# Kernel tuning notes

Measured on AMD Instinct MI355X. Metric: run time of the kernel, lower is better.

## Reference

```python
import jax, jax.numpy as jnp
import numpy as np
from jax import lax

B, IMG, P, C_IN, E, H, NAX = 128, 224, 16, 1, 96, 4, 14
N = NAX * NAX  # 196 patches


def _ln(x, g, b, axes=(-1,)):
    mu = jnp.mean(x, axes, keepdims=True)
    v = jnp.var(x, axes, keepdims=True)
    return (x - mu) * lax.rsqrt(v + 1e-5) * g + b


def _embed3d(p):
    # p: [B, N, E]. Torch code rotates pair (2i,2i+1) by theta_i*col (row loop)
    # then theta_i*row (col loop) in-place => total angle theta_i*(row+col).
    bsz = p.shape[0]
    f = p.transpose(0, 2, 1).reshape(bsz, E, NAX, NAX)
    i = jnp.arange(E // 2, dtype=jnp.float32)
    theta = 10000.0 ** (-2.0 * i / E)  # [48]
    pos = jnp.arange(NAX, dtype=jnp.float32)
    ang = theta[:, None, None] * (pos[None, :, None] + pos[None, None, :])  # [48,14,14]
    cos, sin = jnp.cos(ang), jnp.sin(ang)
    xe, ye = f[:, 0::2], f[:, 1::2]  # [B,48,14,14] each
    rx = xe * cos - ye * sin
    ry = xe * sin + ye * cos
    f = jnp.stack([rx, ry], axis=2).reshape(bsz, E, NAX, NAX)  # re-interleave pairs
    return f.reshape(bsz, E, N).transpose(0, 2, 1)


def _mhsa(x, g, bt, Wqkv, bqkv, Wo, bo):
    # standard pre-norm residual MHSA block (MHSelfAttentionBlock assumed)
    h = _ln(x, g, bt)
    qkv = h @ Wqkv + bqkv  # [B,N,3E]
    q, k, v = jnp.split(qkv, 3, axis=-1)
    d = E // H
    def heads(t):
        return t.reshape(t.shape[0], N, H, d).transpose(0, 2, 1, 3)  # [B,H,N,d]
    q, k, v = heads(q), heads(k), heads(v)
    s = jnp.einsum('bhqd,bhkd->bhqk', q, k) / jnp.sqrt(jnp.float32(d))
    a = jax.nn.softmax(s, axis=-1)
    o = jnp.einsum('bhqk,bhkd->bhqd', a, v).transpose(0, 2, 1, 3).reshape(x.shape[0], N, E)
    return x + o @ Wo + bo


def _convT(x, w, b):
    # torch ConvTranspose2d(k=4, s=2, p=1); w: [C_in, C_out, 4, 4]
    wt = jnp.transpose(jnp.flip(w, (2, 3)), (1, 0, 2, 3))  # OIHW, flipped
    y = lax.conv_general_dilated(x, wt, (1, 1), ((2, 2), (2, 2)), lhs_dilation=(2, 2),
                                 dimension_numbers=('NCHW', 'OIHW', 'NCHW'))
    return y + b[None, :, None, None]


def _forward(x, timestep, Wp, bp, Wt1, bt1, Wt2, bt2,
             a0_g, a0_b, a0_Wqkv, a0_bqkv, a0_Wo, a0_bo,
             a1_g, a1_b, a1_Wqkv, a1_bqkv, a1_Wo, a1_bo,
             Wm0, bm0, Wm1, bm1, Wm2, bm2,
             Wd1, bd1, l1g, l1b, Wd2, bd2, l2g, l2b, Wd3, bd3, l3g, l3b, Wd4, bd4):
    # timestep embedding: emb = -log(0.5)*t -> [sin, cos] -> MLP
    e = 0.6931471805599453 * timestep[0]
    tv = jnp.stack([jnp.sin(e), jnp.cos(e)])  # [2]
    time = jax.nn.silu(tv @ Wt1 + bt1) @ Wt2 + bt2  # [E]
    # patch embed: conv stride 16
    p = lax.conv_general_dilated(x, Wp, (P, P), 'VALID',
                                 dimension_numbers=('NCHW', 'OIHW', 'NCHW'))
    p = (p + bp[None, :, None, None]).reshape(x.shape[0], E, N).transpose(0, 2, 1)  # [B,N,E]
    p = _embed3d(p)
    p = _mhsa(p, a0_g, a0_b, a0_Wqkv, a0_bqkv, a0_Wo, a0_bo)
    p = _mhsa(p, a1_g, a1_b, a1_Wqkv, a1_bqkv, a1_Wo, a1_bo)
    p = p + time
    p = jax.nn.silu(p @ Wm0 + bm0)
    p = jax.nn.silu(p @ Wm1 + bm1)
    p = jax.nn.silu(p @ Wm2 + bm2)
    # unpatchify decoder
    f = p.transpose(0, 2, 1).reshape(x.shape[0], E, NAX, NAX)
    f = jax.nn.silu(_ln(_convT(f, Wd1, bd1), l1g, l1b, (-2, -1)))  # [B,48,28,28]
    f = jax.nn.silu(_ln(_convT(f, Wd2, bd2), l2g, l2b, (-2, -1)))  # [B,24,56,56]
    f = jax.nn.silu(_ln(_convT(f, Wd3, bd3), l3g, l3b, (-2, -1)))  # [B,12,112,112]
    f = jax.nn.silu(_convT(f, Wd4, bd4))                            # [B,1,224,224]
    return jnp.clip(f, 0.0, 1.0)


def setup_inputs() -> dict:
    ks = jax.random.split(jax.random.key(0), 40)
    rn = lambda k, s: (jax.random.normal(k, s, jnp.float32) * 0.02)
    inp = {
        'x': jax.random.normal(ks[0], (B, C_IN, IMG, IMG), jnp.float32),
        'timestep': jax.random.uniform(ks[1], (1,), jnp.float32),
        'Wp': rn(ks[2], (E, C_IN, P, P)), 'bp': jnp.zeros((E,), jnp.float32),
        'Wt1': rn(ks[3], (2, 128)), 'bt1': jnp.zeros((128,), jnp.float32),
        'Wt2': rn(ks[4], (128, E)), 'bt2': jnp.zeros((E,), jnp.float32),
        'a0_g': jnp.ones((E,), jnp.float32), 'a0_b': jnp.zeros((E,), jnp.float32),
        'a0_Wqkv': rn(ks[5], (E, 3 * E)), 'a0_bqkv': jnp.zeros((3 * E,), jnp.float32),
        'a0_Wo': rn(ks[6], (E, E)), 'a0_bo': jnp.zeros((E,), jnp.float32),
        'a1_g': jnp.ones((E,), jnp.float32), 'a1_b': jnp.zeros((E,), jnp.float32),
        'a1_Wqkv': rn(ks[7], (E, 3 * E)), 'a1_bqkv': jnp.zeros((3 * E,), jnp.float32),
        'a1_Wo': rn(ks[8], (E, E)), 'a1_bo': jnp.zeros((E,), jnp.float32),
        'Wm0': rn(ks[9], (E, E)), 'bm0': jnp.zeros((E,), jnp.float32),
        'Wm1': rn(ks[10], (E, E)), 'bm1': jnp.zeros((E,), jnp.float32),
        'Wm2': rn(ks[11], (E, E)), 'bm2': jnp.zeros((E,), jnp.float32),
        'Wd1': rn(ks[12], (E, 48, 4, 4)), 'bd1': jnp.zeros((48,), jnp.float32),
        'l1g': jnp.ones((28, 28), jnp.float32), 'l1b': jnp.zeros((28, 28), jnp.float32),
        'Wd2': rn(ks[13], (48, 24, 4, 4)), 'bd2': jnp.zeros((24,), jnp.float32),
        'l2g': jnp.ones((56, 56), jnp.float32), 'l2b': jnp.zeros((56, 56), jnp.float32),
        'Wd3': rn(ks[14], (24, 12, 4, 4)), 'bd3': jnp.zeros((12,), jnp.float32),
        'l3g': jnp.ones((112, 112), jnp.float32), 'l3b': jnp.zeros((112, 112), jnp.float32),
        'Wd4': rn(ks[15], (12, 1, 4, 4)), 'bd4': jnp.zeros((1,), jnp.float32),
    }
    return inp


def reference(x, timestep, Wp, bp, Wt1, bt1, Wt2, bt2,
              a0_g, a0_b, a0_Wqkv, a0_bqkv, a0_Wo, a0_bo,
              a1_g, a1_b, a1_Wqkv, a1_bqkv, a1_Wo, a1_bo,
              Wm0, bm0, Wm1, bm1, Wm2, bm2,
              Wd1, bd1, l1g, l1b, Wd2, bd2, l2g, l2b, Wd3, bd3, l3g, l3b, Wd4, bd4):
    return _forward(x, timestep, Wp, bp, Wt1, bt1, Wt2, bt2,
                    a0_g, a0_b, a0_Wqkv, a0_bqkv, a0_Wo, a0_bo,
                    a1_g, a1_b, a1_Wqkv, a1_bqkv, a1_Wo, a1_bo,
                    Wm0, bm0, Wm1, bm1, Wm2, bm2,
                    Wd1, bd1, l1g, l1b, Wd2, bd2, l2g, l2b, Wd3, bd3, l3g, l3b, Wd4, bd4)
```

## Files before the change

kernel.cpp:

```cpp
#include <hip/hip_runtime.h>
#include <cmath>


#define B_   128
#define NPATCH 196
#define M_ROWS (B_*NPATCH)
#define E_   96

typedef _Float16 half8 __attribute__((ext_vector_type(8)));
typedef _Float16 half4v __attribute__((ext_vector_type(4)));
typedef _Float16 half2v __attribute__((ext_vector_type(2)));
typedef float f32x4 __attribute__((ext_vector_type(4)));

__global__ void k_time(const float* __restrict__ ts,
                       const float* __restrict__ Wt1, const float* __restrict__ bt1,
                       const float* __restrict__ Wt2, const float* __restrict__ bt2,
                       float* __restrict__ timev)
{
    __shared__ float h[128];
    float e = 0.69314718055994530942f * ts[0];
    float sv = sinf(e), cv = cosf(e);
    int t = threadIdx.x;
    float z = sv * Wt1[t] + cv * Wt1[128 + t] + bt1[t];
    h[t] = z / (1.f + expf(-z));
    __syncthreads();
    if (t < 96) {
        float acc = bt2[t];
        for (int j = 0; j < 128; ++j) acc += h[j] * Wt2[j * 96 + t];
        timev[t] = acc;
    }
}

__global__ void __launch_bounds__(256) k_zstat(float* __restrict__ stat)
{
    int i = blockIdx.x * 256 + threadIdx.x;
    if (i < 21504) stat[i] = 0.f;
}

__global__ void __launch_bounds__(256) k_repack(const float* __restrict__ w1,
                                                const float* __restrict__ w2,
                                                const float* __restrict__ w3,
                                                const float* __restrict__ w4f,
                                                float* __restrict__ wr)
{
    int i = blockIdx.x * 256 + threadIdx.x;
    const float* src; int CIN, COUT, e; float* dst;
    if      (i < 73728) { src = w1;  CIN = 96; COUT = 48; e = i;          dst = wr; }
    else if (i < 92160) { src = w2;  CIN = 48; COUT = 24; e = i - 73728;  dst = wr + 73728; }
    else if (i < 96768) { src = w3;  CIN = 24; COUT = 12; e = i - 92160;  dst = wr + 92160; }
    else if (i < 96960) { src = w4f; CIN = 12; COUT = 1;  e = i - 96768;  dst = wr + 96768; }
    else return;
    int per = CIN * COUT * 4;
    int par = e / per, rem = e % per;
    int ci = rem / (COUT * 4);
    int o  = (rem >> 2) % COUT;
    int j  = rem & 3;
    int ry = par >> 1, rx = par & 1;
    int wy = (j < 2)  ? (3 - ry) : (1 - ry);
    int wx = (j & 1)  ? (1 - rx) : (3 - rx);
    dst[e] = src[(ci * COUT + o) * 16 + wy * 4 + wx];
}

__global__ void k_wcvt4(const float* __restrict__ wr4,
                        _Float16* __restrict__ wcf)
{
    int i = threadIdx.x;
    if (i >= 192) return;
    int p = i / 48, rem = i % 48;
    int j = rem / 12, ci = rem % 12;
    wcf[(p * 4 + j) * 12 + ci] = (_Float16)wr4[p * 48 + ci * 4 + j];
}

__global__ void __launch_bounds__(256) k_wcvtp(const float* __restrict__ Wp,
                                               _Float16* __restrict__ wph)
{
    int i = blockIdx.x * 256 + threadIdx.x;
    if (i >= 24576) return;
    int kc = i / 12288, rem = i % 12288;
    int e = rem / 128, k = rem % 128;
    wph[i] = (_Float16)Wp[e * 256 + kc * 128 + k];
}

__global__ void __launch_bounds__(256) k_wcvtc(const float* __restrict__ w1,
                                               _Float16* __restrict__ wc)
{
    int i = blockIdx.x * 256 + threadIdx.x;
    if (i >= 4 * 48 * 384) return;
    int p = i / 18432, rem = i % 18432;
    int o = rem / 384, k = rem % 384;
    int tap = k / 96, ci = k % 96;
    int ry = p >> 1, rx = p & 1;
    int wy = (tap < 2) ? (3 - ry) : (1 - ry);
    int wx = (tap & 1) ? (1 - rx) : (3 - rx);
    wc[i] = (_Float16)w1[(ci * 48 + o) * 16 + wy * 4 + wx];
}

__global__ void __launch_bounds__(256) k_wcvt2(const float* __restrict__ w2,
                                               _Float16* __restrict__ wc2)
{
    int i = blockIdx.x * 256 + threadIdx.x;
    if (i >= 4 * 32 * 192) return;
    int p = i / 6144, rem = i % 6144;
    int o = rem / 192, k = rem % 192;
    int tap = k / 48, ci = k % 48;
    int ry = p >> 1, rx = p & 1;
    int wy = (tap < 2) ? (3 - ry) : (1 - ry);
    int wx = (tap & 1) ? (1 - rx) : (3 - rx);
    wc2[i] = (o < 24) ? (_Float16)w2[(ci * 24 + o) * 16 + wy * 4 + wx]
                      : (_Float16)0.f;
}

__global__ void __launch_bounds__(256) k_wcvt3(const float* __restrict__ w3,
                                               _Float16* __restrict__ wc3)
{
    int i = blockIdx.x * 256 + threadIdx.x;
    if (i >= 4 * 16 * 96) return;
    int p = i / 1536, rem = i % 1536;
    int o = rem / 96, k = rem % 96;
    int tap = k / 24, ci = k % 24;
    int ry = p >> 1, rx = p & 1;
    int wy = (tap < 2) ? (3 - ry) : (1 - ry);
    int wx = (tap & 1) ? (1 - rx) : (3 - rx);
    wc3[i] = (o < 12) ? (_Float16)w3[(ci * 12 + o) * 16 + wy * 4 + wx]
                      : (_Float16)0.f;
}

__global__ void __launch_bounds__(256) k_wcvt(const float* __restrict__ qkv0,
                                              const float* __restrict__ qkv1,
                                              const float* __restrict__ wo0,
                                              const float* __restrict__ wo1,
                                              const float* __restrict__ wm0,
                                              const float* __restrict__ wm1,
                                              const float* __restrict__ wm2,
                                              _Float16* __restrict__ wh)
{
    int i = blockIdx.x * 256 + threadIdx.x;
    const float* src; int N; int e;
    if      (i < 27648)  { src = qkv0; N = 288; e = i; }
    else if (i < 55296)  { src = qkv1; N = 288; e = i - 27648; }
    else if (i < 64512)  { src = wo0;  N = 96;  e = i - 55296; }
    else if (i < 73728)  { src = wo1;  N = 96;  e = i - 64512; }
    else if (i < 82944)  { src = wm0;  N = 96;  e = i - 73728; }
    else if (i < 92160)  { src = wm1;  N = 96;  e = i - 82944; }
    else if (i < 101376) { src = wm2;  N = 96;  e = i - 92160; }
    else return;
    int n = e / 96, k = e % 96;
    wh[i] = (_Float16)src[k * N + n];
}

__global__ void __launch_bounds__(256) k_zb_h(_Float16* __restrict__ xinh)
{
    int i = blockIdx.x * 256 + threadIdx.x;
    if (i >= 128 * 60 * 96) return;
    int b = i / 5760, r = i % 5760;
    int pos = r / 96, ch = r % 96;
    int py, px;
    if      (pos < 16) { py = 0;        px = pos; }
    else if (pos < 32) { py = 15;       px = pos - 16; }
    else if (pos < 46) { py = pos - 31; px = 0; }
    else               { py = pos - 45; px = 15; }
    xinh[((size_t)(b * 256) + py * 16 + px) * 96 + ch] = (_Float16)0.f;
}

__global__ void __launch_bounds__(256) k_patch_mfma(const float* __restrict__ x,
                                                    const _Float16* __restrict__ wph,
                                                    const float* __restrict__ bp,
                                                    float* __restrict__ out)
{
    __shared__ __align__(16) _Float16 Ah[32 * 136];
    __shared__ __align__(16) _Float16 Wh[96 * 136];
    int t = threadIdx.x;
    int p0 = blockIdx.x * 32;
    int wave = t >> 6, lane = t & 63;
    int lm = lane & 15, quad = lane >> 4;
    int rt = wave >> 1, nh = wave & 1;
    f32x4 acc[3];
    #pragma unroll
    for (int nt = 0; nt < 3; ++nt) acc[nt] = (f32x4){0.f, 0.f, 0.f, 0.f};

    for (int kc = 0; kc < 2; ++kc) {
        __syncthreads();
        {
            int lp = t >> 3, pyl = t & 7;
            int patch = p0 + lp;
            int b = patch / NPATCH, n = patch % NPATCH;
            int ny = n / 14, nx = n % 14;
            const float4* s4 = (const float4*)(x +
                ((size_t)(b * 224) + ny * 16 + kc * 8 + pyl) * 224 + nx * 16);
            float4 v0 = s4[0], v1 = s4[1], v2 = s4[2], v3 = s4[3];
            half8 h0, h1;
            h0[0]=(_Float16)v0.x; h0[1]=(_Float16)v0.y; h0[2]=(_Float16)v0.z; h0[3]=(_Float16)v0.w;
            h0[4]=(_Float16)v1.x; h0[5]=(_Float16)v1.y; h0[6]=(_Float16)v1.z; h0[7]=(_Float16)v1.w;
            h1[0]=(_Float16)v2.x; h1[1]=(_Float16)v2.y; h1[2]=(_Float16)v2.z; h1[3]=(_Float16)v2.w;
            h1[4]=(_Float16)v3.x; h1[5]=(_Float16)v3.y; h1[6]=(_Float16)v3.z; h1[7]=(_Float16)v3.w;
            *(half8*)&Ah[lp * 136 + pyl * 16]     = h0;
            *(half8*)&Ah[lp * 136 + pyl * 16 + 8] = h1;
        }
        {
            const uint4* src = (const uint4*)(wph + (size_t)kc * 12288);
            for (int i = t; i < 1536; i += 256) {
                int e = i >> 4, s = i & 15;
                *(uint4*)&Wh[e * 136 + s * 8] = src[i];
            }
        }
        __syncthreads();
        half8 af[4];
        #pragma unroll
        for (int ks = 0; ks < 4; ++ks)
            af[ks] = *(const half8*)&Ah[(rt * 16 + lm) * 136 + ks * 32 + quad * 8];
        #pragma unroll
        for (int ks = 0; ks < 4; ++ks) {
            #pragma unroll
            for (int nt = 0; nt < 3; ++nt) {
                half8 bf = *(const half8*)&Wh[((nh * 3 + nt) * 16 + lm) * 136 + ks * 32 + quad * 8];
                acc[nt] = __builtin_amdgcn_mfma_f32_16x16x32_f16(af[ks], bf, acc[nt], 0, 0, 0);
            }
        }
    }

    #pragma unroll
    for (int nt = 0; nt < 3; ++nt) {
        #pragma unroll
        for (int r = 0; r < 4; ++r) {
            int e = (nh * 3 + nt) * 16 + lm;
            int lp = rt * 16 + quad * 4 + r;
            int patch = p0 + lp;
            int n = patch % NPATCH;
            int ny = n / 14, nx = n % 14;
            float yx = (float)(ny + nx);
            float v = acc[nt][r] + bp[e];
            float other = __shfl_xor(v, 1);
            float fi = (float)(e >> 1);
            float theta = expf(fi * (-2.f / 96.f) * 9.210340371976184f);
            float ang = theta * yx;
            float c = cosf(ang), s = sinf(ang);
            float outv = (lm & 1) ? (other * s + v * c) : (v * c - other * s);
            out[(size_t)patch * 96 + e] = outv;
        }
    }
}

__global__ void __launch_bounds__(256) k_ln_row(const float* __restrict__ x,
                                                const float* __restrict__ g,
                                                const float* __restrict__ bv,
                                                _Float16* __restrict__ out, int M)
{
    int lane = threadIdx.x & 63;
    int gw = (blockIdx.x * 256 + threadIdx.x) >> 6;
    int nw = (gridDim.x * 256) >> 6;
    float g0 = g[lane], b0 = bv[lane];
    float g1 = 0.f, b1 = 0.f;
    if (lane < 32) { g1 = g[64 + lane]; b1 = bv[64 + lane]; }
    for (int r = gw; r < M; r += nw) {
        const float* xr = x + (size_t)r * 96;
        float a = xr[lane];
        float c = (lane < 32) ? xr[64 + lane] : 0.f;
        float s = a + c, q = a * a + c * c;
        #pragma unroll
        for (int off = 32; off; off >>= 1) {
            s += __shfl_xor(s, off);
            q += __shfl_xor(q, off);
        }
        float mu = s * (1.f / 96.f);
        float rstd = rsqrtf(q * (1.f / 96.f) - mu * mu + 1e-5f);
        _Float16* orow = out + (size_t)r * 96;
        orow[lane] = (_Float16)((a - mu) * rstd * g0 + b0);
        if (lane < 32) orow[64 + lane] = (_Float16)((c - mu) * rstd * g1 + b1);
    }
}

template<int NCHUNKS, int OUTMODE, bool SILU, bool RES, bool ADDTIME, bool AHALF>
__global__ void __launch_bounds__(256) k_gemm_mfma(const void* __restrict__ A,
                                                   const _Float16* __restrict__ Wt,
                                                   const float* __restrict__ bias,
                                                   const float* __restrict__ res,
                                                   const float* __restrict__ timev,
                                                   void* __restrict__ outp)
{
    __shared__ __align__(16) _Float16 Ah[64 * 96];
    __shared__ __align__(16) _Float16 Wh[96 * 96];
    constexpr int NTOT = NCHUNKS * 96;
    int t = threadIdx.x;
    size_t row0 = (size_t)blockIdx.x * 64;

    if constexpr (AHALF) {
        const uint4* a4 = (const uint4*)((const _Float16*)A + row0 * 96);
        uint4* dst = (uint4*)Ah;
        for (int i = t; i < 768; i += 256) dst[i] = a4[i];
    } else {
        const float4* a4 = (const float4*)((const float*)A + row0 * 96);
        for (int i = t; i < 1536; i += 256) {
            float4 v = a4[i];
            half4v hv;
            hv[0] = (_Float16)v.x; hv[1] = (_Float16)v.y;
            hv[2] = (_Float16)v.z; hv[3] = (_Float16)v.w;
            *(half4v*)&Ah[i * 4] = hv;
        }
    }

    int wave = t >> 6, lane = t & 63;
    int lm = lane & 15, quad = lane >> 4;
    const f32x4 vzero = {0.f, 0.f, 0.f, 0.f};

    for (int ch = blockIdx.y; ch < NCHUNKS; ch += gridDim.y) {
        __syncthreads();
        {
            const uint4* src = (const uint4*)(Wt + (size_t)ch * 9216);
            uint4* dst = (uint4*)Wh;
            for (int i = t; i < 1152; i += 256) dst[i] = src[i];
        }
        __syncthreads();

        half8 af[3];
        #pragma unroll
        for (int ks = 0; ks < 3; ++ks)
            af[ks] = *(const half8*)&Ah[(wave * 16 + lm) * 96 + ks * 32 + quad * 8];

        f32x4 acc[6];
        #pragma unroll
        for (int ct = 0; ct < 6; ++ct) acc[ct] = vzero;

        #pragma unroll
        for (int ct = 0; ct < 6; ++ct) {
            #pragma unroll
            for (int ks = 0; ks < 3; ++ks) {
                half8 bf = *(const half8*)&Wh[(ct * 16 + lm) * 96 + ks * 32 + quad * 8];
                acc[ct] = __builtin_amdgcn_mfma_f32_16x16x32_f16(af[ks], bf, acc[ct], 0, 0, 0);
            }
        }

        #pragma unroll
        for (int ct = 0; ct < 6; ++ct) {
            #pragma unroll
            for (int r = 0; r < 4; ++r) {
                int lr = wave * 16 + quad * 4 + r;
                size_t row = row0 + lr;
                int lc = ct * 16 + lm;
                int col = ch * 96 + lc;
                float v = acc[ct][r] + bias[col];
                if constexpr (RES)     v += res[row * 96 + lc];
                if constexpr (ADDTIME) v += timev[lc];
                if constexpr (SILU)    v = v / (1.f + __expf(-v));
                if constexpr (OUTMODE == 0) {
                    ((float*)outp)[row * NTOT + col] = v;
                } else {
                    ((_Float16*)outp)[row * NTOT + col] = (_Float16)v;
                }
            }
        }
    }
}

__global__ void __launch_bounds__(256) k_mlp_fused(const _Float16* __restrict__ A,
                                                   const _Float16* __restrict__ W,
                                                   const float* __restrict__ b0,
                                                   const float* __restrict__ b1,
                                                   const float* __restrict__ b2,
                                                   _Float16* __restrict__ outh)
{
    __shared__ __align__(16) _Float16 Ah[2][64 * 96];
    __shared__ __align__(16) _Float16 Wh[3][96 * 96];
    int t = threadIdx.x;
    size_t row0 = (size_t)blockIdx.x * 64;

    {
        const uint4* a4 = (const uint4*)(A + row0 * 96);
        uint4* dst = (uint4*)&Ah[0][0];
        for (int i = t; i < 768; i += 256) dst[i] = a4[i];
    }
    {
        const uint4* src = (const uint4*)W;
        uint4* dst = (uint4*)&Wh[0][0];
        for (int i = t; i < 3456; i += 256) dst[i] = src[i];
    }

    int wave = t >> 6, lane = t & 63;
    int lm = lane & 15, quad = lane >> 4;
    const float* biases[3] = { b0, b1, b2 };
    int cur = 0;

    #pragma unroll
    for (int s = 0; s < 3; ++s) {
        __syncthreads();
        half8 af[3];
        #pragma unroll
        for (int ks = 0; ks < 3; ++ks)
            af[ks] = *(const half8*)&Ah[cur][(wave * 16 + lm) * 96 + ks * 32 + quad * 8];

        f32x4 acc[6];
        #pragma unroll
        for (int ct = 0; ct < 6; ++ct) acc[ct] = (f32x4){0.f, 0.f, 0.f, 0.f};

        #pragma unroll
        for (int ct = 0; ct < 6; ++ct) {
            #pragma unroll
            for (int ks = 0; ks < 3; ++ks) {
                half8 bf = *(const half8*)&Wh[s][(ct * 16 + lm) * 96 + ks * 32 + quad * 8];
                acc[ct] = __builtin_amdgcn_mfma_f32_16x16x32_f16(af[ks], bf, acc[ct], 0, 0, 0);
            }
        }

        const float* bias = biases[s];
        if (s < 2) {
            #pragma unroll
            for (int ct = 0; ct < 6; ++ct) {
                #pragma unroll
                for (int r = 0; r < 4; ++r) {
                    int lr = wave * 16 + quad * 4 + r;
                    int lc = ct * 16 + lm;
                    float v = acc[ct][r] + bias[lc];
                    v = v / (1.f + __expf(-v));
                    Ah[cur ^ 1][lr * 96 + lc] = (_Float16)v;
                }
            }
            cur ^= 1;
        } else {
            #pragma unroll
            for (int ct = 0; ct < 6; ++ct) {
                #pragma unroll
                for (int r = 0; r < 4; ++r) {
                    int lr = wave * 16 + quad * 4 + r;
                    size_t row = row0 + lr;
                    int lc = ct * 16 + lm;
                    float v = acc[ct][r] + bias[lc];
                    v = v / (1.f + __expf(-v));
                    size_t b = row / NPATCH; int n = (int)(row % NPATCH);
                    int ny = n / 14, nx = n % 14;
                    outh[((b * 256) + (1 + ny) * 16 + (1 + nx)) * 96 + lc] = (_Float16)v;
                }
            }
        }
    }
}

__global__ void __launch_bounds__(256) k_attn_mfma(const _Float16* __restrict__ qkv,
                                                   _Float16* __restrict__ o)
{
    __shared__ __align__(16) _Float16 Qs[208 * 40];
    __shared__ __align__(16) _Float16 Ks[208 * 40];
    __shared__ __align__(16) _Float16 Vt[32 * 232];
    __shared__ __align__(16) _Float16 Pw[4][16 * 232];

    int t = threadIdx.x;
    int bh = blockIdx.x;
    int b = bh >> 2, h = bh & 3;
    const _Float16* base = qkv + (size_t)b * NPATCH * 288 + h * 24;

    {
        const int4 z = {0, 0, 0, 0};
        int4* q4 = (int4*)Qs; int4* k4 = (int4*)Ks;
        for (int i = t; i < 1040; i += 256) { q4[i] = z; k4[i] = z; }
        int4* v4 = (int4*)Vt;
        for (int i = t; i < 928; i += 256) v4[i] = z;
        int4* p4 = (int4*)&Pw[0][0];
        for (int i = t; i < 1856; i += 256) p4[i] = z;
    }
    __syncthreads();

    for (int i = t; i < NPATCH * 24; i += 256) {
        int r = i / 24, d = i % 24;
        const _Float16* row = base + (size_t)r * 288;
        Qs[r * 40 + d]   = row[d];
        Ks[r * 40 + d]   = row[96 + d];
        Vt[d * 232 + r]  = row[192 + d];
    }
    __syncthreads();

    int wave = t >> 6, lane = t & 63;
    int lm = lane & 15, quad = lane >> 4;
    const float scale = 0.2041241452319315f;

    half8 bk[13];
    #pragma unroll
    for (int ct = 0; ct < 13; ++ct)
        bk[ct] = *(const half8*)&Ks[(ct * 16 + lm) * 40 + quad * 8];

    _Float16* pw = &Pw[wave][0];

    for (int rt = wave; rt < 13; rt += 4) {
        half8 aq = *(const half8*)&Qs[(rt * 16 + lm) * 40 + quad * 8];
        float rsum[4] = {0.f, 0.f, 0.f, 0.f};

        #pragma unroll
        for (int ct = 0; ct < 13; ++ct) {
            f32x4 s = (f32x4){0.f, 0.f, 0.f, 0.f};
            s = __builtin_amdgcn_mfma_f32_16x16x32_f16(aq, bk[ct], s, 0, 0, 0);
            #pragma unroll
            for (int r = 0; r < 4; ++r) {
                float p = __expf(fminf(s[r] * scale, 60.f));
                if (ct == 12 && lm >= 4) p = 0.f;
                rsum[r] += p;
                pw[(quad * 4 + r) * 232 + ct * 16 + lm] = (_Float16)p;
            }
        }

        #pragma unroll
        for (int r = 0; r < 4; ++r) {
            float s = rsum[r];
            s += __shfl_xor(s, 1);
            s += __shfl_xor(s, 2);
            s += __shfl_xor(s, 4);
            s += __shfl_xor(s, 8);
            rsum[r] = 1.f / s;
        }

        f32x4 ov0 = (f32x4){0.f, 0.f, 0.f, 0.f};
        f32x4 ov1 = (f32x4){0.f, 0.f, 0.f, 0.f};
        #pragma unroll
        for (int ks = 0; ks < 7; ++ks) {
            half8 ap = *(const half8*)&pw[lm * 232 + ks * 32 + quad * 8];
            half8 bv0 = *(const half8*)&Vt[(lm) * 232 + ks * 32 + quad * 8];
            half8 bv1 = *(const half8*)&Vt[(16 + lm) * 232 + ks * 32 + quad * 8];
            ov0 = __builtin_amdgcn_mfma_f32_16x16x32_f16(ap, bv0, ov0, 0, 0, 0);
            ov1 = __builtin_amdgcn_mfma_f32_16x16x32_f16(ap, bv1, ov1, 0, 0, 0);
        }

        #pragma unroll
        for (int r = 0; r < 4; ++r) {
            int row = rt * 16 + quad * 4 + r;
            if (row < NPATCH) {
                _Float16* orow = o + ((size_t)b * NPATCH + row) * 96 + h * 24;
                orow[lm] = (_Float16)(ov0[r] * rsum[r]);
                if (lm < 8) orow[16 + lm] = (_Float16)(ov1[r] * rsum[r]);
            }
        }
    }
}

__global__ void __launch_bounds__(256) k_conv1_tile(const _Float16* __restrict__ xinh,
                                                    const _Float16* __restrict__ wc,
                                                    const float* __restrict__ bias,
                                                    _Float16* __restrict__ c1,
                                                    float* __restrict__ pstat1)
{
    __shared__ __align__(16) _Float16 Xs[4 * 16 * 104];
    __shared__ float bins[96];
    int t = threadIdx.x;
    int blk = blockIdx.x;
    int b = blk / 7, s = blk % 7;

    if (t < 96) bins[t] = 0.f;

    for (int i = t; i < 768; i += 256) {
        int r = i / 192, rem = i % 192;
        int c = rem / 12, ch = (rem % 12) * 8;
        *(uint4*)&Xs[(r * 16 + c) * 104 + ch] =
            *(const uint4*)(xinh + ((size_t)(b * 256) + (2 * s + r) * 16 + c) * 96 + ch);
    }

    int wave = t >> 6, lane = t & 63;
    int lm = lane & 15, quad = lane >> 4;
    int ry = wave >> 1, rx = wave & 1;

    __syncthreads();

    for (int nt = 0; nt < 3; ++nt) {
        half8 bf[12];
        #pragma unroll
        for (int ks = 0; ks < 12; ++ks)
            bf[ks] = *(const half8*)&wc[((size_t)(wave * 48 + nt * 16 + lm)) * 384
                                        + ks * 32 + quad * 8];

        float sl = 0.f, ql = 0.f;
        #pragma unroll
        for (int rt = 0; rt < 2; ++rt) {
            int pp = rt * 16 + lm;
            int ppc = pp < 28 ? pp : 27;
            int pyl = ppc / 14, px = ppc % 14;

            half8 af[12];
            #pragma unroll
            for (int ks = 0; ks < 12; ++ks) {
                int k0 = ks * 32 + quad * 8;
                int tap = k0 / 96, off = k0 % 96;
                int dy = tap >> 1, dx = tap & 1;
                af[ks] = *(const half8*)&Xs[((pyl + ry + dy) * 16 + (px + rx + dx)) * 104 + off];
            }

            f32x4 acc = (f32x4){0.f, 0.f, 0.f, 0.f};
            #pragma unroll
            for (int ks = 0; ks < 12; ++ks)
                acc = __builtin_amdgcn_mfma_f32_16x16x32_f16(af[ks], bf[ks], acc, 0, 0, 0);

            #pragma unroll
            for (int r = 0; r < 4; ++r) {
                int pw = rt * 16 + quad * 4 + r;
                if (pw < 28) {
                    int pylw = pw / 14, pxw = pw % 14;
                    int oy = 2 * (2 * s + pylw) + ry, ox = 2 * pxw + rx;
                    float v = acc[r] + bias[nt * 16 + lm];
                    sl += v; ql += v * v;
                    c1[((size_t)(b * 28 + oy) * 28 + ox) * 48 + nt * 16 + lm] = (_Float16)v;
                }
            }
        }
        atomicAdd(&bins[(nt * 16 + lm) * 2],     sl);
        atomicAdd(&bins[(nt * 16 + lm) * 2 + 1], ql);
    }
    __syncthreads();
    if (t < 96) atomicAdd(&pstat1[(size_t)b * 96 + t], bins[t]);
}

__global__ void __launch_bounds__(256) k_ln1_apply(const _Float16* __restrict__ c1,
                                                   const float* __restrict__ pstat1,
                                                   const float* __restrict__ g,
                                                   const float* __restrict__ bv,
                                                   _Float16* __restrict__ xh)
{
    int i4 = blockIdx.x * 256 + threadIdx.x;
    int idx = i4 * 4;
    int ch = idx % 48;
    int t2 = idx / 48;
    int pos = t2 % 900;
    int b = t2 / 900;
    int py = pos / 30, px = pos % 30;
    half4v hv = (half4v){(_Float16)0.f, (_Float16)0.f, (_Float16)0.f, (_Float16)0.f};
    if (py >= 1 && py <= 28 && px >= 1 && px <= 28) {
        int j = (py - 1) * 28 + (px - 1);
        half4v v = *(const half4v*)&c1[((size_t)b * 784 + j) * 48 + ch];
        const float* ps = pstat1 + (size_t)b * 96 + ch * 2;
        float gj = g[j], bj = bv[j];
        #pragma unroll
        for (int k = 0; k < 4; ++k) {
            float mu = ps[2 * k] * (1.f / 784.f);
            float rstd = rsqrtf(ps[2 * k + 1] * (1.f / 784.f) - mu * mu + 1e-5f);
            float u = ((float)v[k] - mu) * rstd * gj + bj;
            hv[k] = (_Float16)(u / (1.f + __expf(-u)));
        }
    }
    *(half4v*)&xh[idx] = hv;
}

__global__ void __launch_bounds__(256) k_conv2_tile(const _Float16* __restrict__ xh,
                                                    const _Float16* __restrict__ wc,
                                                    const float* __restrict__ bias,
                                                    _Float16* __restrict__ c2,
                                                    float* __restrict__ pstat2)
{
    __shared__ __align__(16) _Float16 Xs[4 * 30 * 56];
    __shared__ float bins[48];
    int t = threadIdx.x;
    int blk = blockIdx.x;
    int b = blk / 14, s = blk % 14;

    if (t < 48) bins[t] = 0.f;

    for (int i = t; i < 720; i += 256) {
        int r = i / 180, rem = i % 180;
        int c = rem / 6, ch = (rem % 6) * 8;
        *(uint4*)&Xs[(r * 30 + c) * 56 + ch] =
            *(const uint4*)(xh + ((size_t)(b * 900) + (2 * s + r) * 30 + c) * 48 + ch);
    }

    int wave = t >> 6, lane = t & 63;
    int lm = lane & 15, quad = lane >> 4;
    int ry = wave >> 1, rx = wave & 1;

    half8 bf0[6], bf1[6];
    #pragma unroll
    for (int ks = 0; ks < 6; ++ks) {
        bf0[ks] = *(const half8*)&wc[((size_t)(wave * 32 + lm)) * 192 + ks * 32 + quad * 8];
        bf1[ks] = *(const half8*)&wc[((size_t)(wave * 32 + 16 + lm)) * 192 + ks * 32 + quad * 8];
    }

    __syncthreads();

    float s0l = 0.f, q0l = 0.f, s1l = 0.f, q1l = 0.f;
    #pragma unroll
    for (int rt = 0; rt < 4; ++rt) {
        int pp = rt * 16 + lm;
        int ppc = pp < 56 ? pp : 55;
        int pyl = ppc / 28, px = ppc % 28;

        half8 af[6];
        #pragma unroll
        for (int ks = 0; ks < 6; ++ks) {
            int k0 = ks * 32 + quad * 8;
            int tap = k0 / 48, off = k0 % 48;
            int dy = tap >> 1, dx = tap & 1;
            af[ks] = *(const half8*)&Xs[((pyl + ry + dy) * 30 + (px + rx + dx)) * 56 + off];
        }

        f32x4 acc0 = (f32x4){0.f, 0.f, 0.f, 0.f};
        f32x4 acc1 = (f32x4){0.f, 0.f, 0.f, 0.f};
        #pragma unroll
        for (int ks = 0; ks < 6; ++ks) {
            acc0 = __builtin_amdgcn_mfma_f32_16x16x32_f16(af[ks], bf0[ks], acc0, 0, 0, 0);
            acc1 = __builtin_amdgcn_mfma_f32_16x16x32_f16(af[ks], bf1[ks], acc1, 0, 0, 0);
        }

        #pragma unroll
        for (int r = 0; r < 4; ++r) {
            int pw = rt * 16 + quad * 4 + r;
            if (pw < 56) {
                int pylw = pw / 28, pxw = pw % 28;
                int oy = 2 * (2 * s + pylw) + ry, ox = 2 * pxw + rx;
                _Float16* orow = c2 + ((size_t)(b * 56 + oy) * 56 + ox) * 24;
                float v0 = acc0[r] + bias[lm];
                orow[lm] = (_Float16)v0;
                s0l += v0; q0l += v0 * v0;
                if (lm < 8) {
                    float v1 = acc1[r] + bias[16 + lm];
                    orow[16 + lm] = (_Float16)v1;
                    s1l += v1; q1l += v1 * v1;
                }
            }
        }
    }
    atomicAdd(&bins[lm * 2],     s0l);
    atomicAdd(&bins[lm * 2 + 1], q0l);
    if (lm < 8) {
        atomicAdd(&bins[(16 + lm) * 2],     s1l);
        atomicAdd(&bins[(16 + lm) * 2 + 1], q1l);
    }
    __syncthreads();
    if (t < 48) atomicAdd(&pstat2[(size_t)b * 48 + t], bins[t]);
}

__global__ void __launch_bounds__(256) k_ln2_apply(const _Float16* __restrict__ c2,
                                                   const float* __restrict__ pstat2,
                                                   const float* __restrict__ g,
                                                   const float* __restrict__ bv,
                                                   _Float16* __restrict__ xh)
{
    int i4 = blockIdx.x * 256 + threadIdx.x;
    int idx = i4 * 4;
    int ch = idx % 24;
    int t2 = idx / 24;
    int pos = t2 % 3364;
    int b = t2 / 3364;
    int py = pos / 58, px = pos % 58;
    half4v hv = (half4v){(_Float16)0.f, (_Float16)0.f, (_Float16)0.f, (_Float16)0.f};
    if (py >= 1 && py <= 56 && px >= 1 && px <= 56) {
        int j = (py - 1) * 56 + (px - 1);
        half4v v = *(const half4v*)&c2[((size_t)b * 3136 + j) * 24 + ch];
        const float* ps = pstat2 + (size_t)b * 48 + ch * 2;
        float gj = g[j], bj = bv[j];
        #pragma unroll
        for (int k = 0; k < 4; ++k) {
            float mu = ps[2 * k] * (1.f / 3136.f);
            float rstd = rsqrtf(ps[2 * k + 1] * (1.f / 3136.f) - mu * mu + 1e-5f);
            float u = ((float)v[k] - mu) * rstd * gj + bj;
            hv[k] = (_Float16)(u / (1.f + __expf(-u)));
        }
    }
    *(half4v*)&xh[idx] = hv;
}

__global__ void __launch_bounds__(256) k_conv3_tile(const _Float16* __restrict__ xh,
                                                    const _Float16* __restrict__ wc,
                                                    const float* __restrict__ bias,
                                                    _Float16* __restrict__ c3,
                                                    float* __restrict__ pstat3)
{
    __shared__ __align__(16) _Float16 Xs[3 * 58 * 40];
    __shared__ float bins[24];
    int t = threadIdx.x;
    int blk = blockIdx.x;
    int b = blk / 56, s = blk % 56;

    if (t < 24) bins[t] = 0.f;

    for (int i = t; i < 522; i += 256) {
        int r = i / 174, rem = i % 174;
        int c = rem / 3, ch = (rem % 3) * 8;
        *(uint4*)&Xs[(r * 58 + c) * 40 + ch] =
            *(const uint4*)(xh + ((size_t)(b * 3364) + (s + r) * 58 + c) * 24 + ch);
    }

    int wave = t >> 6, lane = t & 63;
    int lm = lane & 15, quad = lane >> 4;
    int ry = wave >> 1, rx = wave & 1;

    half8 bf[3];
    #pragma unroll
    for (int ks = 0; ks < 3; ++ks)
        bf[ks] = *(const half8*)&wc[((size_t)(wave * 16 + lm)) * 96 + ks * 32 + quad * 8];

    __syncthreads();

    float sl = 0.f, ql = 0.f;
    #pragma unroll
    for (int rt = 0; rt < 4; ++rt) {
        int px = rt * 16 + lm;
        int pxc = px < 56 ? px : 55;

        half8 af[3];
        #pragma unroll
        for (int ks = 0; ks < 3; ++ks) {
            int k0 = ks * 32 + quad * 8;
            int tap = k0 / 24, off = k0 % 24;
            int dy = tap >> 1, dx = tap & 1;
            af[ks] = *(const half8*)&Xs[((ry + dy) * 58 + (pxc + rx + dx)) * 40 + off];
        }

        f32x4 acc = (f32x4){0.f, 0.f, 0.f, 0.f};
        #pragma unroll
        for (int ks = 0; ks < 3; ++ks)
            acc = __builtin_amdgcn_mfma_f32_16x16x32_f16(af[ks], bf[ks], acc, 0, 0, 0);

        if (lm < 12) {
            #pragma unroll
            for (int r = 0; r < 4; ++r) {
                int pw = rt * 16 + quad * 4 + r;
                if (pw < 56) {
                    int oy = 2 * s + ry, ox = 2 * pw + rx;
                    float v = acc[r] + bias[lm];
                    sl += v; ql += v * v;
                    c3[((size_t)(b * 112 + oy) * 112 + ox) * 12 + lm] = (_Float16)v;
                }
            }
        }
    }
    if (lm < 12) {
        atomicAdd(&bins[lm * 2],     sl);
        atomicAdd(&bins[lm * 2 + 1], ql);
    }
    __syncthreads();
    if (t < 24) atomicAdd(&pstat3[(size_t)b * 24 + t], bins[t]);
}

__global__ void __launch_bounds__(256) k_ln3_apply(const _Float16* __restrict__ c3,
                                                   const float* __restrict__ pstat3,
                                                   const float* __restrict__ g,
                                                   const float* __restrict__ bv,
                                                   _Float16* __restrict__ xh4)
{
    int i4 = blockIdx.x * 256 + threadIdx.x;
    int idx = i4 * 4;
    int ch = idx % 12;
    int t2 = idx / 12;
    int pix = t2 % 12544;
    int b = t2 / 12544;
    half4v v = *(const half4v*)&c3[idx];
    const float* ps = pstat3 + (size_t)b * 24 + ch * 2;
    float gp = g[pix], bp = bv[pix];
    half4v hv;
    #pragma unroll
    for (int k = 0; k < 4; ++k) {
        float mu = ps[2 * k] * (1.f / 12544.f);
        float rstd = rsqrtf(ps[2 * k + 1] * (1.f / 12544.f) - mu * mu + 1e-5f);
        float u = ((float)v[k] - mu) * rstd * gp + bp;
        hv[k] = (_Float16)(u / (1.f + __expf(-u)));
    }
    *(half4v*)&xh4[idx] = hv;
}

__global__ void __launch_bounds__(256) k_conv_final3(const _Float16* __restrict__ x,
                                                     const _Float16* __restrict__ wcf,
                                                     const float* __restrict__ bias,
                                                     float* __restrict__ out)
{
    constexpr int HIN = 112, CIN = 12;
    __shared__ __align__(16) _Float16 Xs[4 * 114 * 12];
    __shared__ __align__(16) _Float16 Wl[192];
    int t = threadIdx.x;
    int blk = blockIdx.x;
    int b = blk / 56, s = blk % 56;
    int py0 = 2 * s;

    {
        const int4 z = {0, 0, 0, 0};
        int4* p4 = (int4*)Xs;
        for (int i = t; i < 684; i += 256) p4[i] = z;
        if (t < 24) *(int4*)&Wl[t * 8] = *(const int4*)&wcf[t * 8];
    }
    __syncthreads();
    for (int i = t; i < 672; i += 256) {
        int r = i / 168, rem = i % 168;
        int row = py0 - 1 + r;
        if (row >= 0 && row < HIN) {
            *(uint4*)&Xs[(size_t)r * 1368 + rem * 8] =
                *(const uint4*)(x + ((size_t)b * HIN * HIN + (size_t)row * HIN) * CIN + rem * 8);
        }
    }
    __syncthreads();

    if (t >= 224) return;
    int pyl = t / 112;
    int px = t % 112;
    int py = py0 + pyl;

    half2v tvp[9][6];
    #pragma unroll
    for (int a = 0; a < 3; ++a) {
        int lr = pyl + a;
        #pragma unroll
        for (int c = 0; c < 3; ++c) {
            int col = px - 1 + c;
            int cs = (col < 0) ? 113 : col;
            const _Float16* p = &Xs[((size_t)lr * 114 + cs) * 12];
            half4v h0 = *(const half4v*)&p[0];
            half4v h1 = *(const half4v*)&p[4];
            half4v h2 = *(const half4v*)&p[8];
            int ti = a * 3 + c;
            tvp[ti][0] = (half2v){h0[0], h0[1]};
            tvp[ti][1] = (half2v){h0[2], h0[3]};
            tvp[ti][2] = (half2v){h1[0], h1[1]};
            tvp[ti][3] = (half2v){h1[2], h1[3]};
            tvp[ti][4] = (half2v){h2[0], h2[1]};
            tvp[ti][5] = (half2v){h2[2], h2[3]};
        }
    }

    float bb = bias[0];
    float* ob = out + (size_t)b * 50176;
    #pragma unroll
    for (int ry = 0; ry < 2; ++ry) {
        float res[2];
        #pragma unroll
        for (int rx = 0; rx < 2; ++rx) {
            int p = ry * 2 + rx;
            float acc = 0.f;
            #pragma unroll
            for (int dy = 0; dy < 2; ++dy) {
                #pragma unroll
                for (int dx = 0; dx < 2; ++dx) {
                    int j = dy * 2 + dx;
                    int ti = (ry + dy) * 3 + (rx + dx);
                    const half2v* wp = (const half2v*)&Wl[(p * 4 + j) * 12];
                    #pragma unroll
                    for (int k = 0; k < 6; ++k)
                        acc = __builtin_amdgcn_fdot2(tvp[ti][k], wp[k], acc, false);
                }
            }
            float u = acc + bb;
            u = u / (1.f + __expf(-u));
            res[rx] = fminf(fmaxf(u, 0.f), 1.f);
        }
        float2 v; v.x = res[0]; v.y = res[1];
        *(float2*)(ob + (size_t)(2 * py + ry) * 224 + 2 * px) = v;
    }
}

extern "C" void kernel_launch(void* const* d_in, const int* in_sizes, int n_in,
                              void* d_out, int out_size, void* d_ws, size_t ws_size,
                              hipStream_t stream)
{
    const float* x       = (const float*)d_in[0];
    const float* ts      = (const float*)d_in[1];
    const float* Wp      = (const float*)d_in[2];
    const float* bp      = (const float*)d_in[3];
    const float* Wt1     = (const float*)d_in[4];
    const float* bt1     = (const float*)d_in[5];
    const float* Wt2     = (const float*)d_in[6];
    const float* bt2     = (const float*)d_in[7];
    const float* a0_g    = (const float*)d_in[8];
    const float* a0_b    = (const float*)d_in[9];
    const float* a0_Wqkv = (const float*)d_in[10];
    const float* a0_bqkv = (const float*)d_in[11];
    const float* a0_Wo   = (const float*)d_in[12];
    const float* a0_bo   = (const float*)d_in[13];
    const float* a1_g    = (const float*)d_in[14];
    const float* a1_b    = (const float*)d_in[15];
    const float* a1_Wqkv = (const float*)d_in[16];
    const float* a1_bqkv = (const float*)d_in[17];
    const float* a1_Wo   = (const float*)d_in[18];
    const float* a1_bo   = (const float*)d_in[19];
    const float* Wm0     = (const float*)d_in[20];
    const float* bm0     = (const float*)d_in[21];
    const float* Wm1     = (const float*)d_in[22];
    const float* bm1     = (const float*)d_in[23];
    const float* Wm2     = (const float*)d_in[24];
    const float* bm2     = (const float*)d_in[25];
    const float* Wd1     = (const float*)d_in[26];
    const float* bd1     = (const float*)d_in[27];
    const float* l1g     = (const float*)d_in[28];
    const float* l1b     = (const float*)d_in[29];
    const float* Wd2     = (const float*)d_in[30];
    const float* bd2     = (const float*)d_in[31];
    const float* l2g     = (const float*)d_in[32];
    const float* l2b     = (const float*)d_in[33];
    const float* Wd3     = (const float*)d_in[34];
    const float* bd3     = (const float*)d_in[35];
    const float* l3g     = (const float*)d_in[36];
    const float* l3b     = (const float*)d_in[37];
    const float* Wd4     = (const float*)d_in[38];
    const float* bd4     = (const float*)d_in[39];
    float* out = (float*)d_out;

    const size_t R = 2408448;
    float* ws   = (float*)d_ws;
    float* tvec = ws;
    float* p0   = ws + 512;
    _Float16* p0h  = (_Float16*)(ws + 512);
    _Float16* hh   = (_Float16*)(ws + 512 + R);
    _Float16* qkvh = (_Float16*)(ws + 512 + 2 * R);
    _Float16* obh  = (_Float16*)(ws + 512 + 5 * R);
    float* p1   = ws + 512 + 6 * R;
    _Float16* xinh = (_Float16*)(ws + 512 + 2 * R);
    _Float16* C1h  = (_Float16*)(ws + 512 + 5 * R);
    _Float16* xh2  = (_Float16*)(ws + 512 + 7 * R);
    _Float16* C2h  = (_Float16*)(ws + 512);
    _Float16* xh3  = (_Float16*)(ws + 512 + 7 * R + 5529600);
    _Float16* C3h  = (_Float16*)(ws + 512);
    _Float16* xh4  = (_Float16*)(ws + 512 + 7 * R + 5529600);
    float* Wr   = ws + 512 + 7 * R + 5529600 + 10334208;
    _Float16* WH = (_Float16*)(Wr + 96960);
    _Float16* Wc  = (_Float16*)Wr;
    _Float16* Wc2 = (_Float16*)(Wr + 36864);
    _Float16* Wc3 = (_Float16*)(Wr + 49152);
    float* stat = Wr + 96960 + 50688;
    float* stat1 = stat;
    float* stat2 = stat + 12288;
    float* stat3 = stat + 18432;
    _Float16* Wcf = (_Float16*)(stat + 21504);
    _Float16* Wph = (_Float16*)(stat + 21504 + 128);
    const size_t NEED = (512 + 7 * R + 5529600 + 10334208 + 96960 + 50688 + 21504
                         + 128 + 12288 + 16) * sizeof(float);
    if (ws_size < NEED) return;

    _Float16* WHqkv0 = WH;
    _Float16* WHqkv1 = WH + 27648;
    _Float16* WHwo0  = WH + 55296;
    _Float16* WHwo1  = WH + 64512;
    _Float16* WHwm0  = WH + 73728;

    k_time<<<1, 128, 0, stream>>>(ts, Wt1, bt1, Wt2, bt2, tvec);
    k_zstat<<<84, 256, 0, stream>>>(stat);
    k_repack<<<379, 256, 0, stream>>>(Wd1, Wd2, Wd3, Wd4, Wr);
    k_wcvt4<<<1, 192, 0, stream>>>(Wr + 96768, Wcf);
    k_wcvtp<<<96, 256, 0, stream>>>(Wp, Wph);
    k_wcvtc<<<288, 256, 0, stream>>>(Wd1, Wc);
    k_wcvt2<<<96, 256, 0, stream>>>(Wd2, Wc2);
    k_wcvt3<<<24, 256, 0, stream>>>(Wd3, Wc3);
    k_wcvt<<<396, 256, 0, stream>>>(a0_Wqkv, a1_Wqkv, a0_Wo, a1_Wo,
                                    Wm0, Wm1, Wm2, WH);
    k_patch_mfma<<<M_ROWS / 32, 256, 0, stream>>>(x, Wph, bp, p0);

    k_ln_row<<<1024, 256, 0, stream>>>(p0, a0_g, a0_b, hh, M_ROWS);
    k_gemm_mfma<3, 1, false, false, false, true><<<dim3(M_ROWS / 64, 3), 256, 0, stream>>>(
        hh, WHqkv0, a0_bqkv, nullptr, nullptr, qkvh);
    k_attn_mfma<<<B_ * 4, 256, 0, stream>>>(qkvh, obh);
    k_gemm_mfma<1, 0, false, true, false, true><<<dim3(M_ROWS / 64, 1), 256, 0, stream>>>(
        obh, WHwo0, a0_bo, p0, nullptr, p1);

    k_ln_row<<<1024, 256, 0, stream>>>(p1, a1_g, a1_b, hh, M_ROWS);
    k_gemm_mfma<3, 1, false, false, false, true><<<dim3(M_ROWS / 64, 3), 256, 0, stream>>>(
        hh, WHqkv1, a1_bqkv, nullptr, nullptr, qkvh);
    k_attn_mfma<<<B_ * 4, 256, 0, stream>>>(qkvh, obh);
    k_gemm_mfma<1, 1, false, true, true, true><<<dim3(M_ROWS / 64, 1), 256, 0, stream>>>(
        obh, WHwo1, a1_bo, p1, tvec, p0h);

    k_zb_h<<<2880, 256, 0, stream>>>(xinh);

    k_mlp_fused<<<M_ROWS / 64, 256, 0, stream>>>(p0h, WHwm0, bm0, bm1, bm2, xinh);

    k_conv1_tile<<<B_ * 7, 256, 0, stream>>>(xinh, Wc, bd1, C1h, stat1);
    k_ln1_apply<<<5400, 256, 0, stream>>>(C1h, stat1, l1g, l1b, xh2);
    k_conv2_tile<<<B_ * 14, 256, 0, stream>>>(xh2, Wc2, bd2, C2h, stat2);
    k_ln2_apply<<<10092, 256, 0, stream>>>(C2h, stat2, l2g, l2b, xh3);
    k_conv3_tile<<<B_ * 56, 256, 0, stream>>>(xh3, Wc3, bd3, C3h, stat3);
    k_ln3_apply<<<18816, 256, 0, stream>>>(C3h, stat3, l3g, l3b, xh4);
    k_conv_final3<<<7168, 256, 0, stream>>>(xh4, Wcf, bd4, out);
}
```

Measured before the change: 431.0 us.

## Fuse LayerNorm+SiLU apply into the following transposed-conv tile loaders

Removes the three standalone LN-apply kernels. Each conv tile kernel now reads the raw previous conv output plus its per-sample statistics and applies LayerNorm and SiLU while staging the tile into shared memory, writing zeros for the padding border. This avoids writing and re-reading the padded normalized activation buffers and saves three launches. In exchange, overlapping halo rows are normalized redundantly and the staging loops do more arithmetic. Workspace aliasing also changes: C3h moves to a separate region so it no longer overlaps C2h.

```diff
diff --git a/kernel.cpp b/kernel.cpp
--- a/kernel.cpp
+++ b/kernel.cpp
@@ -601,37 +601,10 @@
     if (t < 96) atomicAdd(&pstat1[(size_t)b * 96 + t], bins[t]);
 }
 
-__global__ void __launch_bounds__(256) k_ln1_apply(const _Float16* __restrict__ c1,
-                                                   const float* __restrict__ pstat1,
-                                                   const float* __restrict__ g,
-                                                   const float* __restrict__ bv,
-                                                   _Float16* __restrict__ xh)
-{
-    int i4 = blockIdx.x * 256 + threadIdx.x;
-    int idx = i4 * 4;
-    int ch = idx % 48;
-    int t2 = idx / 48;
-    int pos = t2 % 900;
-    int b = t2 / 900;
-    int py = pos / 30, px = pos % 30;
-    half4v hv = (half4v){(_Float16)0.f, (_Float16)0.f, (_Float16)0.f, (_Float16)0.f};
-    if (py >= 1 && py <= 28 && px >= 1 && px <= 28) {
-        int j = (py - 1) * 28 + (px - 1);
-        half4v v = *(const half4v*)&c1[((size_t)b * 784 + j) * 48 + ch];
-        const float* ps = pstat1 + (size_t)b * 96 + ch * 2;
-        float gj = g[j], bj = bv[j];
-        #pragma unroll
-        for (int k = 0; k < 4; ++k) {
-            float mu = ps[2 * k] * (1.f / 784.f);
-            float rstd = rsqrtf(ps[2 * k + 1] * (1.f / 784.f) - mu * mu + 1e-5f);
-            float u = ((float)v[k] - mu) * rstd * gj + bj;
-            hv[k] = (_Float16)(u / (1.f + __expf(-u)));
-        }
-    }
-    *(half4v*)&xh[idx] = hv;
-}
-
-__global__ void __launch_bounds__(256) k_conv2_tile(const _Float16* __restrict__ xh,
+__global__ void __launch_bounds__(256) k_conv2_tile(const _Float16* __restrict__ c1,
+                                                    const float* __restrict__ pstat1,
+                                                    const float* __restrict__ g1,
+                                                    const float* __restrict__ b1v,
                                                     const _Float16* __restrict__ wc,
                                                     const float* __restrict__ bias,
                                                     _Float16* __restrict__ c2,
@@ -647,9 +620,26 @@
 
     for (int i = t; i < 720; i += 256) {
         int r = i / 180, rem = i % 180;
-        int c = rem / 6, ch = (rem % 6) * 8;
-        *(uint4*)&Xs[(r * 30 + c) * 56 + ch] =
-            *(const uint4*)(xh + ((size_t)(b * 900) + (2 * s + r) * 30 + c) * 48 + ch);
+        int c = rem / 6, ch0 = (rem % 6) * 8;
+        int py = 2 * s + r, px = c;
+        half8 hv;
+        if (py >= 1 && py <= 28 && px >= 1 && px <= 28) {
+            int j = (py - 1) * 28 + (px - 1);
+            half8 v = *(const half8*)&c1[((size_t)b * 784 + j) * 48 + ch0];
+            const float* ps = pstat1 + (size_t)b * 96 + ch0 * 2;
+            float gj = g1[j], bj = b1v[j];
+            #pragma unroll
+            for (int k = 0; k < 8; ++k) {
+                float mu = ps[2 * k] * (1.f / 784.f);
+                float rstd = rsqrtf(ps[2 * k + 1] * (1.f / 784.f) - mu * mu + 1e-5f);
+                float u = ((float)v[k] - mu) * rstd * gj + bj;
+                hv[k] = (_Float16)(u / (1.f + __expf(-u)));
+            }
+        } else {
+            #pragma unroll
+            for (int k = 0; k < 8; ++k) hv[k] = (_Float16)0.f;
+        }
+        *(half8*)&Xs[(r * 30 + c) * 56 + ch0] = hv;
     }
 
     int wave = t >> 6, lane = t & 63;
@@ -717,37 +707,10 @@
     if (t < 48) atomicAdd(&pstat2[(size_t)b * 48 + t], bins[t]);
 }
 
-__global__ void __launch_bounds__(256) k_ln2_apply(const _Float16* __restrict__ c2,
-                                                   const float* __restrict__ pstat2,
-                                                   const float* __restrict__ g,
-                                                   const float* __restrict__ bv,
-                                                   _Float16* __restrict__ xh)
-{
-    int i4 = blockIdx.x * 256 + threadIdx.x;
-    int idx = i4 * 4;
-    int ch = idx % 24;
-    int t2 = idx / 24;
-    int pos = t2 % 3364;
-    int b = t2 / 3364;
-    int py = pos / 58, px = pos % 58;
-    half4v hv = (half4v){(_Float16)0.f, (_Float16)0.f, (_Float16)0.f, (_Float16)0.f};
-    if (py >= 1 && py <= 56 && px >= 1 && px <= 56) {
-        int j = (py - 1) * 56 + (px - 1);
-        half4v v = *(const half4v*)&c2[((size_t)b * 3136 + j) * 24 + ch];
-        const float* ps = pstat2 + (size_t)b * 48 + ch * 2;
-        float gj = g[j], bj = bv[j];
-        #pragma unroll
-        for (int k = 0; k < 4; ++k) {
-            float mu = ps[2 * k] * (1.f / 3136.f);
-            float rstd = rsqrtf(ps[2 * k + 1] * (1.f / 3136.f) - mu * mu + 1e-5f);
-            float u = ((float)v[k] - mu) * rstd * gj + bj;
-            hv[k] = (_Float16)(u / (1.f + __expf(-u)));
-        }
-    }
-    *(half4v*)&xh[idx] = hv;
-}
-
-__global__ void __launch_bounds__(256) k_conv3_tile(const _Float16* __restrict__ xh,
+__global__ void __launch_bounds__(256) k_conv3_tile(const _Float16* __restrict__ c2,
+                                                    const float* __restrict__ pstat2,
+                                                    const float* __restrict__ g2,
+                                                    const float* __restrict__ b2v,
                                                     const _Float16* __restrict__ wc,
                                                     const float* __restrict__ bias,
                                                     _Float16* __restrict__ c3,
@@ -763,9 +726,26 @@
 
     for (int i = t; i < 522; i += 256) {
         int r = i / 174, rem = i % 174;
-        int c = rem / 3, ch = (rem % 3) * 8;
-        *(uint4*)&Xs[(r * 58 + c) * 40 + ch] =
-            *(const uint4*)(xh + ((size_t)(b * 3364) + (s + r) * 58 + c) * 24 + ch);
+        int c = rem / 3, ch0 = (rem % 3) * 8;
+        int py = s + r, px = c;
+        half8 hv;
+        if (py >= 1 && py <= 56 && px >= 1 && px <= 56) {
+            int j = (py - 1) * 56 + (px - 1);
+            half8 v = *(const half8*)&c2[((size_t)b * 3136 + j) * 24 + ch0];
+            const float* ps = pstat2 + (size_t)b * 48 + ch0 * 2;
+            float gj = g2[j], bj = b2v[j];
+            #pragma unroll
+            for (int k = 0; k < 8; ++k) {
+                float mu = ps[2 * k] * (1.f / 3136.f);
+                float rstd = rsqrtf(ps[2 * k + 1] * (1.f / 3136.f) - mu * mu + 1e-5f);
+                float u = ((float)v[k] - mu) * rstd * gj + bj;
+                hv[k] = (_Float16)(u / (1.f + __expf(-u)));
+            }
+        } else {
+            #pragma unroll
+            for (int k = 0; k < 8; ++k) hv[k] = (_Float16)0.f;
+        }
+        *(half8*)&Xs[(r * 58 + c) * 40 + ch0] = hv;
     }
 
     int wave = t >> 6, lane = t & 63;
@@ -820,33 +800,10 @@
     if (t < 24) atomicAdd(&pstat3[(size_t)b * 24 + t], bins[t]);
 }
 
-__global__ void __launch_bounds__(256) k_ln3_apply(const _Float16* __restrict__ c3,
-                                                   const float* __restrict__ pstat3,
-                                                   const float* __restrict__ g,
-                                                   const float* __restrict__ bv,
-                                                   _Float16* __restrict__ xh4)
-{
-    int i4 = blockIdx.x * 256 + threadIdx.x;
-    int idx = i4 * 4;
-    int ch = idx % 12;
-    int t2 = idx / 12;
-    int pix = t2 % 12544;
-    int b = t2 / 12544;
-    half4v v = *(const half4v*)&c3[idx];
-    const float* ps = pstat3 + (size_t)b * 24 + ch * 2;
-    float gp = g[pix], bp = bv[pix];
-    half4v hv;
-    #pragma unroll
-    for (int k = 0; k < 4; ++k) {
-        float mu = ps[2 * k] * (1.f / 12544.f);
-        float rstd = rsqrtf(ps[2 * k + 1] * (1.f / 12544.f) - mu * mu + 1e-5f);
-        float u = ((float)v[k] - mu) * rstd * gp + bp;
-        hv[k] = (_Float16)(u / (1.f + __expf(-u)));
-    }
-    *(half4v*)&xh4[idx] = hv;
-}
-
-__global__ void __launch_bounds__(256) k_conv_final3(const _Float16* __restrict__ x,
+__global__ void __launch_bounds__(256) k_conv_final3(const _Float16* __restrict__ c3,
+                                                     const float* __restrict__ pstat3,
+                                                     const float* __restrict__ g3,
+                                                     const float* __restrict__ b3v,
                                                      const _Float16* __restrict__ wcf,
                                                      const float* __restrict__ bias,
                                                      float* __restrict__ out)
@@ -866,12 +823,43 @@
         if (t < 24) *(int4*)&Wl[t * 8] = *(const int4*)&wcf[t * 8];
     }
     __syncthreads();
-    for (int i = t; i < 672; i += 256) {
-        int r = i / 168, rem = i % 168;
+    if (t < 224) {
+        int r = t / 56, u = t % 56;
         int row = py0 - 1 + r;
         if (row >= 0 && row < HIN) {
-            *(uint4*)&Xs[(size_t)r * 1368 + rem * 8] =
-                *(const uint4*)(x + ((size_t)b * HIN * HIN + (size_t)row * HIN) * CIN + rem * 8);
+            size_t base = ((size_t)b * 12544 + (size_t)row * 112 + 2 * u) * 12;
+            half4v v0 = *(const half4v*)&c3[base];
+            half4v v1 = *(const half4v*)&c3[base + 4];
+            half4v v2 = *(const half4v*)&c3[base + 8];
+            half4v v3 = *(const half4v*)&c3[base + 12];
+            half4v v4 = *(const half4v*)&c3[base + 16];
+            half4v v5 = *(const half4v*)&c3[base + 20];
+            int j0 = row * 112 + 2 * u;
+            float ga = g3[j0], ba = b3v[j0];
+            float gb = g3[j0 + 1], bb2 = b3v[j0 + 1];
+            const float* ps = pstat3 + (size_t)b * 24;
+            _Float16 ov[24];
+            #pragma unroll
+            for (int k = 0; k < 24; ++k) {
+                int ch = (k < 12) ? k : k - 12;
+                float mu = ps[2 * ch] * (1.f / 12544.f);
+                float rstd = rsqrtf(ps[2 * ch + 1] * (1.f / 12544.f) - mu * mu + 1e-5f);
+                float vv;
+                if      (k < 4)  vv = (float)v0[k];
+                else if (k < 8)  vv = (float)v1[k - 4];
+                else if (k < 12) vv = (float)v2[k - 8];
+                else if (k < 16) vv = (float)v3[k - 12];
+                else if (k < 20) vv = (float)v4[k - 16];
+                else             vv = (float)v5[k - 20];
+                float gk = (k < 12) ? ga : gb;
+                float bk = (k < 12) ? ba : bb2;
+                float u2 = (vv - mu) * rstd * gk + bk;
+                ov[k] = (_Float16)(u2 / (1.f + __expf(-u2)));
+            }
+            _Float16* dst = &Xs[(size_t)r * 1368 + u * 24];
+            *(half8*)&dst[0]  = *(half8*)&ov[0];
+            *(half8*)&dst[8]  = *(half8*)&ov[8];
+            *(half8*)&dst[16] = *(half8*)&ov[16];
         }
     }
     __syncthreads();
@@ -990,11 +978,8 @@
     float* p1   = ws + 512 + 6 * R;
     _Float16* xinh = (_Float16*)(ws + 512 + 2 * R);
     _Float16* C1h  = (_Float16*)(ws + 512 + 5 * R);
-    _Float16* xh2  = (_Float16*)(ws + 512 + 7 * R);
     _Float16* C2h  = (_Float16*)(ws + 512);
-    _Float16* xh3  = (_Float16*)(ws + 512 + 7 * R + 5529600);
-    _Float16* C3h  = (_Float16*)(ws + 512);
-    _Float16* xh4  = (_Float16*)(ws + 512 + 7 * R + 5529600);
+    _Float16* C3h  = (_Float16*)(ws + 512 + 7 * R + 5529600);
     float* Wr   = ws + 512 + 7 * R + 5529600 + 10334208;
     _Float16* WH = (_Float16*)(Wr + 96960);
     _Float16* Wc  = (_Float16*)Wr;
@@ -1047,10 +1032,7 @@
     k_mlp_fused<<<M_ROWS / 64, 256, 0, stream>>>(p0h, WHwm0, bm0, bm1, bm2, xinh);
 
     k_conv1_tile<<<B_ * 7, 256, 0, stream>>>(xinh, Wc, bd1, C1h, stat1);
-    k_ln1_apply<<<5400, 256, 0, stream>>>(C1h, stat1, l1g, l1b, xh2);
-    k_conv2_tile<<<B_ * 14, 256, 0, stream>>>(xh2, Wc2, bd2, C2h, stat2);
-    k_ln2_apply<<<10092, 256, 0, stream>>>(C2h, stat2, l2g, l2b, xh3);
-    k_conv3_tile<<<B_ * 56, 256, 0, stream>>>(xh3, Wc3, bd3, C3h, stat3);
-    k_ln3_apply<<<18816, 256, 0, stream>>>(C3h, stat3, l3g, l3b, xh4);
-    k_conv_final3<<<7168, 256, 0, stream>>>(xh4, Wcf, bd4, out);
-}
+    k_conv2_tile<<<B_ * 14, 256, 0, stream>>>(C1h, stat1, l1g, l1b, Wc2, bd2, C2h, stat2);
+    k_conv3_tile<<<B_ * 56, 256, 0, stream>>>(C2h, stat2, l2g, l2b, Wc3, bd3, C3h, stat3);
+    k_conv_final3<<<7168, 256, 0, stream>>>(C3h, stat3, l3g, l3b, Wcf, bd4, out);
+}
```

After: 428.2 us. Within noise of the previous version (-0.6%).
